# Kernel tuning notes

Measured on AMD Instinct MI355X. Metric: run time of the kernel, lower is better.

Reference implementation:

```python
import jax, jax.numpy as jnp
import numpy as np

B, S, HID, NH = 2, 2048, 2048, 16
HD = HID // NH  # 128
BASE = 10000.0


def rope_tables(seq_len, head_dim):
    inv_freq = 1.0 / (BASE ** (jnp.arange(0, head_dim, 2, dtype=jnp.float32) / head_dim))
    t = jnp.arange(seq_len, dtype=jnp.float32)
    freqs = jnp.einsum('i,j->ij', t, inv_freq)        # [s, d/2]
    emb = jnp.concatenate([freqs, freqs], axis=-1)     # [s, d]
    return jnp.cos(emb), jnp.sin(emb)


def apply_rotary(x, cos, sin):
    # x: [b, s, h, d]; cos/sin: [s, d]
    x1, x2 = x[..., ::2], x[..., 1::2]
    c = cos[None, :, None, ::2]
    s = sin[None, :, None, ::2]
    x1r = x1 * c - x2 * s
    x2r = x1 * s + x2 * c
    return jnp.stack([x1r, x2r], axis=-1).reshape(x.shape)


def setup_inputs() -> dict:
    key = jax.random.key(0)
    ks = jax.random.split(key, 5)
    scale = 1.0 / np.sqrt(HID)
    hidden_states = jax.random.normal(ks[0], (B, S, HID), jnp.float32)
    Wq = jax.random.normal(ks[1], (HID, HID), jnp.float32) * scale
    Wk = jax.random.normal(ks[2], (HID, HID), jnp.float32) * scale
    Wv = jax.random.normal(ks[3], (HID, HID), jnp.float32) * scale
    Wo = jax.random.normal(ks[4], (HID, HID), jnp.float32) * scale
    causal = jnp.tril(jnp.ones((S, S), dtype=bool))
    attention_mask = jnp.where(causal, 0.0, -1e9).astype(jnp.float32)[None, :, :]  # [1, S, S]
    return {'hidden_states': hidden_states, 'Wq': Wq, 'Wk': Wk, 'Wv': Wv,
            'Wo': Wo, 'attention_mask': attention_mask}


def reference(hidden_states, Wq, Wk, Wv, Wo, attention_mask):
    b, s, hid = hidden_states.shape
    q = (hidden_states @ Wq.T).reshape(b, s, NH, HD)
    k = (hidden_states @ Wk.T).reshape(b, s, NH, HD)
    v = (hidden_states @ Wv.T).reshape(b, s, NH, HD)
    cos, sin = rope_tables(s, HD)
    q = apply_rotary(q, cos, sin)
    k = apply_rotary(k, cos, sin)
    # [b, h, s, d]
    q = q.transpose(0, 2, 1, 3)
    k = k.transpose(0, 2, 1, 3)
    v = v.transpose(0, 2, 1, 3)
    scores = jnp.einsum('bhqd,bhkd->bhqk', q, k) / np.sqrt(HD).astype(np.float32)
    scores = scores + attention_mask[:, None, :, :]  # broadcast mask over heads
    probs = jax.nn.softmax(scores.astype(jnp.float32), axis=-1).astype(q.dtype)
    attn = jnp.einsum('bhqk,bhkd->bhqd', probs, v)
    attn = attn.transpose(0, 2, 1, 3).reshape(b, s, hid)
    return attn @ Wo.T
```

## Files before the change

kernel.cpp:

```cpp
#include <hip/hip_runtime.h>
#include <math.h>

typedef __attribute__((ext_vector_type(8))) short short8;
typedef __attribute__((ext_vector_type(4))) float f32x4;
typedef __attribute__((ext_vector_type(16))) float f32x16;
typedef __attribute__((ext_vector_type(4))) float fvec4;
typedef __attribute__((ext_vector_type(4))) unsigned short us4;
typedef __attribute__((ext_vector_type(2))) unsigned int uint2v;

#define DI __device__ __forceinline__
#define BARX asm volatile("s_barrier" ::: "memory")
#define WAITV6 asm volatile("s_waitcnt vmcnt(6)" ::: "memory")
#define WAITV4 asm volatile("s_waitcnt vmcnt(4)" ::: "memory")
#define WAITV0 asm volatile("s_waitcnt vmcnt(0)" ::: "memory")
#define WAITL0 asm volatile("s_waitcnt lgkmcnt(0)" ::: "memory")
#define SCHED0 __builtin_amdgcn_sched_barrier(0)

constexpr int BB = 2, SS = 2048, HIDc = 2048, NHc = 16, HDc = 128;
constexpr int MT = BB * SS;
constexpr int KC = HIDc;

constexpr size_t OFF_HB  = 0;
constexpr size_t OFF_WB  = OFF_HB + (size_t)MT * KC * 2;
constexpr size_t OFF_Q   = OFF_WB + (size_t)4 * HIDc * KC * 2;
constexpr size_t OFF_K   = OFF_Q  + (size_t)BB * NHc * SS * HDc * 2;
constexpr size_t OFF_V   = OFF_K  + (size_t)BB * NHc * SS * HDc * 2;
constexpr size_t OFF_ATT = OFF_V  + (size_t)BB * NHc * SS * HDc * 2;
constexpr size_t OFF_COS = OFF_ATT + (size_t)MT * HIDc * 2;
constexpr size_t OFF_SIN = OFF_COS + (size_t)SS * 32 * 4;
constexpr size_t WS_NEED = OFF_SIN + (size_t)SS * 32 * 4;

DI float bf2f(unsigned short u) { union { unsigned u; float f; } v; v.u = (unsigned)u << 16; return v.f; }
DI unsigned short f2bf(float f) {
  union { float f; unsigned u; } v; v.f = f;
  unsigned r = v.u + 0x7fffu + ((v.u >> 16) & 1u);
  return (unsigned short)(r >> 16);
}

DI void gload_lds16(const void* g, void* l) {
  __builtin_amdgcn_global_load_lds((const __attribute__((address_space(1))) void*)g,
                                   (__attribute__((address_space(3))) void*)l, 16, 0, 0);
}

DI unsigned cvtpk_bf16(float lo, float hi_) {
  unsigned r;
  asm("v_cvt_pk_bf16_f32 %0, %1, %2" : "=v"(r) : "v"(lo), "v"(hi_));
  return r;
}

__global__ void __launch_bounds__(256) cvt_kernel(
    const float* __restrict__ H,  const float* __restrict__ W0,
    const float* __restrict__ W1, const float* __restrict__ W2,
    const float* __restrict__ W3, unsigned short* __restrict__ dst,
    float* __restrict__ cosT, float* __restrict__ sinT)
{
  constexpr size_t HN = (size_t)MT * KC;
  constexpr size_t WN = (size_t)HIDc * KC;
  if (blockIdx.x >= 12288) {
    int idx = (blockIdx.x - 12288) * 256 + threadIdx.x;
    int t = idx >> 5, fi = idx & 31;
    float inv = powf(10000.0f, -(float)fi * (1.0f / 32.0f));
    float ang = (float)t * inv;
    cosT[idx] = cosf(ang);
    sinT[idx] = sinf(ang);
    return;
  }
  size_t e0 = ((size_t)blockIdx.x * 256 + threadIdx.x) * 8;
  const float* src; size_t off;
  if (e0 < HN) { src = H; off = e0; }
  else {
    size_t t = e0 - HN; int a = (int)(t >> 22);
    src = (a == 0) ? W0 : (a == 1) ? W1 : (a == 2) ? W2 : W3;
    off = t & (WN - 1);
  }
  fvec4 v0 = *(const fvec4*)(src + off);
  fvec4 v1 = *(const fvec4*)(src + off + 4);
  short8 o;
  o[0] = (short)f2bf(v0[0]); o[1] = (short)f2bf(v0[1]);
  o[2] = (short)f2bf(v0[2]); o[3] = (short)f2bf(v0[3]);
  o[4] = (short)f2bf(v1[0]); o[5] = (short)f2bf(v1[1]);
  o[6] = (short)f2bf(v1[2]); o[7] = (short)f2bf(v1[3]);
  *(short8*)(dst + e0) = o;
}

template<int NBX>
__global__ void __launch_bounds__(512, 2) gemm8p(
    const unsigned short* __restrict__ A,
    const unsigned short* __restrict__ Bw,
    void* __restrict__ dq, void* __restrict__ dk, void* __restrict__ dv,
    const float* __restrict__ cosT, const float* __restrict__ sinT)
{
  __shared__ __align__(16) unsigned short SL[8][128 * 64];
  const int tid = threadIdx.x, lane = tid & 63, w = tid >> 6;
  const int wm = w >> 2, wn = w & 3;
  const int ln15 = lane & 15, lq = lane >> 4;

  const int xcd = blockIdx.x & 7, idx = blockIdx.x >> 3;
  const int by = xcd * 2 + idx / NBX, bx = idx % NBX;
  const int m0 = by * 256, n0 = bx * 256;

  const int srow = tid >> 3;
  const int sc = (tid & 7) ^ (srow & 7);
  const unsigned short* Ab = A  + ((size_t)m0 + srow) * KC + sc * 8;
  const unsigned short* Bb = Bw + ((size_t)n0 + srow) * KC + sc * 8;

  constexpr int NT = KC / 64;
  auto stage = [&](int kt, bool isA, int half, int buf) {
    if (kt >= NT) return;
    const unsigned short* s = (isA ? Ab : Bb) + (size_t)(half * 128) * KC + kt * 64;
    int slot = (isA ? 0 : 4) + buf * 2 + half;
    unsigned short* d = &SL[slot][(size_t)(w * 64) * 8];
    gload_lds16(s, d);
    gload_lds16(s + (size_t)64 * KC, d + (size_t)512 * 8);
  };

  auto readA = [&](int buf, int q, int i, int ks) -> short8 {
    int rl = ((q & 1) << 6) + (i << 5) + (wm << 4) + ln15;
    return *(const short8*)&SL[buf * 2 + (q >> 1)]
        [rl * 64 + ((((ks << 2) + lq) ^ (rl & 7)) << 3)];
  };
  auto readB = [&](int buf, int j, int ks) -> short8 {
    int rl = ((wn & 1) << 6) + (j << 4) + ln15;
    return *(const short8*)&SL[4 + buf * 2 + (wn >> 1)]
        [rl * 64 + ((((ks << 2) + lq) ^ (rl & 7)) << 3)];
  };

  stage(0, true, 0, 0); stage(0, true, 1, 0);
  stage(0, false, 0, 0); stage(0, false, 1, 0);
  stage(1, false, 0, 1); stage(1, false, 1, 1); stage(1, true, 0, 1);
  WAITV6; BARX;

  f32x4 acc[8][4] = {};
  short8 bfr[4][2];
  constexpr int NIT = NT / 2;
  for (int t = 0; t < NIT; ++t) {
    const int k2 = 2 * t + 2, k3 = 2 * t + 3;
#pragma unroll
    for (int b = 0; b < 2; ++b) {
#pragma unroll
      for (int q = 0; q < 4; ++q) {
        short8 af[2][2];
#pragma unroll
        for (int i = 0; i < 2; ++i)
#pragma unroll
          for (int ks = 0; ks < 2; ++ks) af[i][ks] = readA(b, q, i, ks);
        if (q == 0) {
#pragma unroll
          for (int j = 0; j < 4; ++j)
#pragma unroll
            for (int ks = 0; ks < 2; ++ks) bfr[j][ks] = readB(b, j, ks);
        }
        if (b == 0) {
          if (q == 0) stage(2 * t + 1, true, 1, 1);
          else if (q == 1) stage(k2, false, 0, 0);
          else if (q == 2) stage(k2, false, 1, 0);
          else stage(k2, true, 0, 0);
        } else {
          if (q == 0) stage(k2, true, 1, 0);
          else if (q == 1) stage(k3, false, 0, 1);
          else if (q == 2) stage(k3, false, 1, 1);
          else stage(k3, true, 0, 1);
        }
        BARX;
        WAITL0; SCHED0;
        __builtin_amdgcn_s_setprio(1);
#pragma unroll
        for (int i = 0; i < 2; ++i)
#pragma unroll
          for (int j = 0; j < 4; ++j)
#pragma unroll
            for (int ks = 0; ks < 2; ++ks)
              acc[2 * q + i][j] = __builtin_amdgcn_mfma_f32_16x16x32_bf16(
                  af[i][ks], bfr[j][ks], acc[2 * q + i][j], 0, 0, 0);
        __builtin_amdgcn_s_setprio(0);
        if (q == 3) { if (t == NIT - 1) { WAITV0; } else { WAITV6; } }
        BARX;
      }
    }
  }

#pragma unroll
  for (int f = 0; f < 8; ++f)
#pragma unroll
    for (int j = 0; j < 4; ++j) {
      int col = n0 + wn * 64 + j * 16 + ln15;
      int z = col >> 11;
      int c2 = col & 2047;
      int h = c2 >> 7, d = c2 & 127;
      int m = m0 + 32 * f + 16 * wm + lq * 4;
      int b = m >> 11, s = m & 2047;
      if (z == 2) {
        us4 pk;
#pragma unroll
        for (int r = 0; r < 4; ++r) pk[r] = f2bf(acc[f][j][r]);
        *(us4*)((unsigned short*)dv + (((size_t)b * NHc + h) * HDc + d) * SS + s) = pk;
      } else {
        unsigned short* D = (unsigned short*)(z ? dk : dq);
        const int fi = (d >> 1) & 31;
        const bool odd = (d & 1) != 0;
#pragma unroll
        for (int r = 0; r < 4; ++r) {
          float v = acc[f][j][r];
          float p = __shfl_xor(v, 1);
          float cs = cosT[(size_t)(s + r) * 32 + fi];
          float sn = sinT[(size_t)(s + r) * 32 + fi];
          float y = odd ? (p * sn + v * cs) : (v * cs - p * sn);
          D[(((size_t)b * NHc + h) * SS + s + r) * HDc + d] = f2bf(y);
        }
      }
    }
}

template<int EPI, int NBX>
__global__ void __launch_bounds__(512, 2) gemm8(
    const unsigned short* __restrict__ A,
    const unsigned short* __restrict__ Bw,
    void* __restrict__ dq, void* __restrict__ dk, void* __restrict__ dv,
    const float* __restrict__ cosT, const float* __restrict__ sinT)
{
  __shared__ __align__(16) unsigned short Al[3][256 * 64];
  __shared__ __align__(16) unsigned short Bl[3][128 * 64];
  const int tid = threadIdx.x, lane = tid & 63, w = tid >> 6;
  const int wm = w >> 1, wn = w & 1;
  const int ln15 = lane & 15, lq = lane >> 4;

  const int xcd = blockIdx.x & 7, idx = blockIdx.x >> 3;
  const int by = xcd * 2 + idx / NBX, bx = idx % NBX;
  const int m0 = by * 256, n0 = bx * 128;

  const int srow = tid >> 3;
  const int sc = (tid & 7) ^ (srow & 7);
  const unsigned short* asrc[4];
  const unsigned short* bsrc[2];
#pragma unroll
  for (int l = 0; l < 4; ++l) asrc[l] = A  + (size_t)(m0 + l * 64 + srow) * KC + sc * 8;
#pragma unroll
  for (int l = 0; l < 2; ++l) bsrc[l] = Bw + (size_t)(n0 + l * 64 + srow) * KC + sc * 8;

  const int x7 = ln15 & 7;
  const int slA0 = (lq ^ x7) * 8;
  const int slA1 = ((4 + lq) ^ x7) * 8;
  int rA[4], rB[4];
#pragma unroll
  for (int i = 0; i < 4; ++i) rA[i] = (wm * 64 + i * 16 + ln15) * 64;
#pragma unroll
  for (int j = 0; j < 4; ++j) rB[j] = (wn * 64 + j * 16 + ln15) * 64;

  constexpr int NT = KC / 64;
  auto stA = [&](int kt, int buf, int l) {
    gload_lds16(asrc[l] + (size_t)kt * 64, &Al[buf][(size_t)(l * 512 + w * 64) * 8]);
  };
  auto stB = [&](int kt, int buf, int l) {
    gload_lds16(bsrc[l] + (size_t)kt * 64, &Bl[buf][(size_t)(l * 512 + w * 64) * 8]);
  };

  stA(0, 0, 0); stA(0, 0, 1); stA(0, 0, 2); stA(0, 0, 3); stB(0, 0, 0); stB(0, 0, 1);
  stA(1, 1, 0); stA(1, 1, 1); stA(1, 1, 2); stA(1, 1, 3); stB(1, 1, 0); stB(1, 1, 1);
  WAITV6; BARX;

  f32x4 acc[4][4] = {};
  int cb = 0, nb = 2;
  for (int kt = 0; kt < NT; ++kt) {
    const unsigned short* Ac = &Al[cb][0];
    const unsigned short* Bc = &Bl[cb][0];
    const bool pf = (kt + 2 < NT);
    short8 a01[2][2], a23[2][2], bf[4][2];

#pragma unroll
    for (int i = 0; i < 2; ++i) {
      a01[i][0] = *(const short8*)&Ac[rA[i] + slA0];
      a01[i][1] = *(const short8*)&Ac[rA[i] + slA1];
    }
#pragma unroll
    for (int j = 0; j < 4; ++j) {
      bf[j][0] = *(const short8*)&Bc[rB[j] + slA0];
      bf[j][1] = *(const short8*)&Bc[rB[j] + slA1];
    }
    if (pf) { stA(kt + 2, nb, 0); stA(kt + 2, nb, 1); stA(kt + 2, nb, 2); }
    BARX;
    WAITL0; SCHED0;
    __builtin_amdgcn_s_setprio(1);
#pragma unroll
    for (int i = 0; i < 2; ++i)
#pragma unroll
      for (int j = 0; j < 4; ++j)
#pragma unroll
        for (int k = 0; k < 2; ++k)
          acc[i][j] = __builtin_amdgcn_mfma_f32_16x16x32_bf16(a01[i][k], bf[j][k], acc[i][j], 0, 0, 0);
    __builtin_amdgcn_s_setprio(0);
    BARX;

#pragma unroll
    for (int i = 0; i < 2; ++i) {
      a23[i][0] = *(const short8*)&Ac[rA[2 + i] + slA0];
      a23[i][1] = *(const short8*)&Ac[rA[2 + i] + slA1];
    }
    if (pf) { stA(kt + 2, nb, 3); stB(kt + 2, nb, 0); stB(kt + 2, nb, 1); }
    BARX;
    WAITL0; SCHED0;
    __builtin_amdgcn_s_setprio(1);
#pragma unroll
    for (int i = 0; i < 2; ++i)
#pragma unroll
      for (int j = 0; j < 4; ++j)
#pragma unroll
        for (int k = 0; k < 2; ++k)
          acc[2 + i][j] = __builtin_amdgcn_mfma_f32_16x16x32_bf16(a23[i][k], bf[j][k], acc[2 + i][j], 0, 0, 0);
    __builtin_amdgcn_s_setprio(0);
    if (kt < NT - 2) { WAITV6; }
    else if (kt == NT - 2) { WAITV0; }
    BARX;

    cb = (cb == 2) ? 0 : cb + 1;
    nb = (nb == 2) ? 0 : nb + 1;
  }

  if (EPI == 1) {
    float* O = (float*)dq;
#pragma unroll
    for (int i = 0; i < 4; ++i)
#pragma unroll
      for (int j = 0; j < 4; ++j) {
        int col = n0 + wn * 64 + j * 16 + ln15;
        int m = m0 + wm * 64 + i * 16 + lq * 4;
#pragma unroll
        for (int r = 0; r < 4; ++r)
          O[(size_t)(m + r) * HIDc + col] = acc[i][j][r];
      }
  } else {
    unsigned short* V = (unsigned short*)dq;
#pragma unroll
    for (int i = 0; i < 4; ++i)
#pragma unroll
      for (int j = 0; j < 4; ++j) {
        int col = n0 + wn * 64 + j * 16 + ln15;
        int h = col >> 7, d = col & 127;
        int m = m0 + wm * 64 + i * 16 + lq * 4;
        int b = m >> 11, s = m & 2047;
        us4 pk;
#pragma unroll
        for (int r = 0; r < 4; ++r) pk[r] = f2bf(acc[i][j][r]);
        *(us4*)(V + (((size_t)b * NHc + h) * HDc + d) * SS + s) = pk;
      }
  }
}

__global__ void __launch_bounds__(512, 2) attn_kernel(
    const unsigned short* __restrict__ Qg,
    const unsigned short* __restrict__ Kg,
    const unsigned short* __restrict__ Vg,
    unsigned short* __restrict__ Og)
{
  __shared__ __align__(16) unsigned short Klds[3][64 * 128];
  __shared__ __align__(16) unsigned short Vlds[3][128 * 64];
  __shared__ __align__(16) unsigned short Plds[8][32 * 64];
  const int tid = threadIdx.x, lane = tid & 63, w = tid >> 6;
  const int l31 = lane & 31, hi = lane >> 5;

  const int wg = blockIdx.x;
  const int xcd = wg & 7, idx = wg >> 3;
  const int bh = xcd + 8 * (idx & 3);
  const int tt = idx >> 2;

  const int qtile = (w < 2) ? tt : (w < 4) ? (tt + 8) : (w < 6) ? (31 - tt) : (23 - tt);
  const int sub1 = w & 1;
  const int q0w = qtile * 64 + sub1 * 32;
  const int ntiles = 32 - tt;

  const size_t hbase = (size_t)bh * SS * HDc;
  const float CE = 1.44269504089f * 0.08838834764831845f;
  const int b = bh >> 4, h = bh & 15;

  short8 qf[8];
#pragma unroll
  for (int ks = 0; ks < 8; ++ks)
    qf[ks] = *(const short8*)(Qg + hbase + (size_t)(q0w + l31) * HDc + ks * 16 + hi * 8);

  f32x16 accO[4];
#pragma unroll
  for (int db = 0; db < 4; ++db)
#pragma unroll
    for (int r = 0; r < 16; ++r) accO[db][r] = 0.f;
  float mr = -1e30f, lr = 0.f;

  auto stage = [&](int kvt, int buf) {
    const int kv0 = kvt * 64;
#pragma unroll
    for (int p = 0; p < 2; ++p) {
      int c = p * 512 + tid;
      int krow = c >> 4, ksl = c & 15;
      gload_lds16(Kg + hbase + (size_t)(kv0 + krow) * HDc + ((ksl ^ (krow & 7)) << 3),
                  (unsigned short*)&Klds[buf][0] + (size_t)c * 8);
      int vd = c >> 3, vsl = c & 7;
      gload_lds16(Vg + hbase + (size_t)vd * SS + kv0 + ((vsl ^ (vd & 7)) << 3),
                  (unsigned short*)&Vlds[buf][0] + (size_t)c * 8);
    }
  };

  stage(0, 0); stage(1, 1);
  WAITV4; BARX;

  for (int kvt = 0; kvt < ntiles; ++kvt) {
    if (kvt + 2 < ntiles) stage(kvt + 2, (kvt + 2) % 3);
    const int cur = kvt % 3;

    if (kvt <= qtile) {
      const bool diag = (kvt == qtile);
      const bool haveT1 = (!diag) || sub1;

      f32x16 s0, s1;
#pragma unroll
      for (int r = 0; r < 16; ++r) s0[r] = 0.f;
      __builtin_amdgcn_s_setprio(1);
#pragma unroll
      for (int ks = 0; ks < 8; ++ks) {
        int row = l31;
        short8 kf = *(const short8*)&Klds[cur][row * 128 + (((2 * ks + hi) ^ (row & 7)) << 3)];
        s0 = __builtin_amdgcn_mfma_f32_32x32x16_bf16(kf, qf[ks], s0, 0, 0, 0);
      }
      if (haveT1) {
#pragma unroll
        for (int r = 0; r < 16; ++r) s1[r] = 0.f;
#pragma unroll
        for (int ks = 0; ks < 8; ++ks) {
          int row = 32 + l31;
          short8 kf = *(const short8*)&Klds[cur][row * 128 + (((2 * ks + hi) ^ (row & 7)) << 3)];
          s1 = __builtin_amdgcn_mfma_f32_32x32x16_bf16(kf, qf[ks], s1, 0, 0, 0);
        }
      }
      __builtin_amdgcn_s_setprio(0);

      if (diag) {
        if (sub1) {
#pragma unroll
          for (int r = 0; r < 16; ++r)
            if (((r & 3) + 8 * (r >> 2) + 4 * hi) > l31) s1[r] = -1e30f;
        } else {
#pragma unroll
          for (int r = 0; r < 16; ++r)
            if (((r & 3) + 8 * (r >> 2) + 4 * hi) > l31) s0[r] = -1e30f;
        }
      }

      float pmax = s0[0];
#pragma unroll
      for (int r = 1; r < 16; ++r) pmax = fmaxf(pmax, s0[r]);
      if (haveT1) {
#pragma unroll
        for (int r = 0; r < 16; ++r) pmax = fmaxf(pmax, s1[r]);
      }
      pmax = fmaxf(pmax, __shfl_xor(pmax, 32));

      int grow = (CE * (pmax - mr) > 8.0f) ? 1 : 0;
      if (__any(grow)) {
        float mn = fmaxf(mr, pmax);
        float al = exp2f(CE * (mr - mn));
        mr = mn; lr *= al;
        float alr[16];
#pragma unroll
        for (int r = 0; r < 16; ++r)
          alr[r] = __shfl(al, (r & 3) + 8 * (r >> 2) + 4 * hi);
#pragma unroll
        for (int db = 0; db < 4; ++db)
#pragma unroll
          for (int r = 0; r < 16; ++r) accO[db][r] *= alr[r];
      }

      float psum = 0.f;
#pragma unroll
      for (int r = 0; r < 16; ++r) {
        float p = exp2f(CE * (s0[r] - mr));
        s0[r] = p; psum += p;
      }
      if (haveT1) {
#pragma unroll
        for (int r = 0; r < 16; ++r) {
          float p = exp2f(CE * (s1[r] - mr));
          s1[r] = p; psum += p;
        }
      }
      psum += __shfl_xor(psum, 32);
      lr += psum;

#pragma unroll
      for (int i = 0; i < 4; ++i) {
        uint2v pk;
        pk[0] = cvtpk_bf16(s0[4 * i], s0[4 * i + 1]);
        pk[1] = cvtpk_bf16(s0[4 * i + 2], s0[4 * i + 3]);
        int chunk = i ^ (l31 & 7);
        *(uint2v*)&Plds[w][l31 * 64 + chunk * 8 + hi * 4] = pk;
      }
      if (haveT1) {
#pragma unroll
        for (int i = 0; i < 4; ++i) {
          uint2v pk;
          pk[0] = cvtpk_bf16(s1[4 * i], s1[4 * i + 1]);
          pk[1] = cvtpk_bf16(s1[4 * i + 2], s1[4 * i + 3]);
          int chunk = (4 + i) ^ (l31 & 7);
          *(uint2v*)&Plds[w][l31 * 64 + chunk * 8 + hi * 4] = pk;
        }
      }

      short8 ap[4];
#pragma unroll
      for (int ks = 0; ks < 2; ++ks)
        ap[ks] = *(const short8*)&Plds[w][l31 * 64 + (((2 * ks + hi) ^ (l31 & 7)) << 3)];
      if (haveT1) {
#pragma unroll
        for (int ks = 2; ks < 4; ++ks)
          ap[ks] = *(const short8*)&Plds[w][l31 * 64 + (((2 * ks + hi) ^ (l31 & 7)) << 3)];
      }

      __builtin_amdgcn_s_setprio(1);
#pragma unroll
      for (int db = 0; db < 4; ++db) {
        int row = db * 32 + l31;
#pragma unroll
        for (int ks = 0; ks < 2; ++ks) {
          short8 vf = *(const short8*)&Vlds[cur][row * 64 + (((2 * ks + hi) ^ (row & 7)) << 3)];
          accO[db] = __builtin_amdgcn_mfma_f32_32x32x16_bf16(ap[ks], vf, accO[db], 0, 0, 0);
        }
      }
      if (haveT1) {
#pragma unroll
        for (int db = 0; db < 4; ++db) {
          int row = db * 32 + l31;
#pragma unroll
          for (int ks = 2; ks < 4; ++ks) {
            short8 vf = *(const short8*)&Vlds[cur][row * 64 + (((2 * ks + hi) ^ (row & 7)) << 3)];
            accO[db] = __builtin_amdgcn_mfma_f32_32x32x16_bf16(ap[ks], vf, accO[db], 0, 0, 0);
          }
        }
      }
      __builtin_amdgcn_s_setprio(0);
    }

    if (kvt < ntiles - 2) { WAITV4; } else { WAITV0; }
    BARX;
  }

  float il = 1.0f / lr;
  float ilr[16];
#pragma unroll
  for (int r = 0; r < 16; ++r)
    ilr[r] = __shfl(il, (r & 3) + 8 * (r >> 2) + 4 * hi);
#pragma unroll
  for (int db = 0; db < 4; ++db)
#pragma unroll
    for (int r = 0; r < 16; ++r) {
      int q = q0w + (r & 3) + 8 * (r >> 2) + 4 * hi;
      int d = db * 32 + l31;
      Og[((size_t)b * SS + q) * HIDc + h * HDc + d] = f2bf(accO[db][r] * ilr[r]);
    }
}

extern "C" void kernel_launch(void* const* d_in, const int* in_sizes, int n_in,
                              void* d_out, int out_size, void* d_ws, size_t ws_size,
                              hipStream_t stream)
{
  if (ws_size < WS_NEED) return;

  const float* H  = (const float*)d_in[0];
  const float* Wq = (const float*)d_in[1];
  const float* Wk = (const float*)d_in[2];
  const float* Wv = (const float*)d_in[3];
  const float* Wo = (const float*)d_in[4];
  char* ws = (char*)d_ws;
  unsigned short* HB = (unsigned short*)(ws + OFF_HB);
  unsigned short* WB = (unsigned short*)(ws + OFF_WB);
  unsigned short* Qb = (unsigned short*)(ws + OFF_Q);
  unsigned short* Kb = (unsigned short*)(ws + OFF_K);
  unsigned short* Vb = (unsigned short*)(ws + OFF_V);
  unsigned short* AT = (unsigned short*)(ws + OFF_ATT);
  float* cosT = (float*)(ws + OFF_COS);
  float* sinT = (float*)(ws + OFF_SIN);

  cvt_kernel<<<12544, 256, 0, stream>>>(H, Wq, Wk, Wv, Wo, HB, cosT, sinT);
  gemm8p<16><<<256, 512, 0, stream>>>(HB, WB, Qb, Kb, Vb, cosT, sinT);
  gemm8<2, 16><<<256, 512, 0, stream>>>(HB, WB + (size_t)2 * HIDc * KC,
                                        Vb, nullptr, nullptr, nullptr, nullptr);
  attn_kernel<<<256, 512, 0, stream>>>(Qb, Kb, Vb, AT);
  gemm8<1, 16><<<256, 512, 0, stream>>>(AT, WB + (size_t)3 * HIDc * KC,
                                        d_out, nullptr, nullptr, nullptr, nullptr);
}
```

Before: 243.6 us.

## Stage 128-row KV tiles double-buffered and split P@V into 32-column halves

```diff
diff --git a/kernel.cpp b/kernel.cpp
--- a/kernel.cpp
+++ b/kernel.cpp
@@ -11,7 +11,6 @@
 #define DI __device__ __forceinline__
 #define BARX asm volatile("s_barrier" ::: "memory")
 #define WAITV6 asm volatile("s_waitcnt vmcnt(6)" ::: "memory")
-#define WAITV4 asm volatile("s_waitcnt vmcnt(4)" ::: "memory")
 #define WAITV0 asm volatile("s_waitcnt vmcnt(0)" ::: "memory")
 #define WAITL0 asm volatile("s_waitcnt lgkmcnt(0)" ::: "memory")
 #define SCHED0 __builtin_amdgcn_sched_barrier(0)
@@ -351,9 +350,9 @@
     const unsigned short* __restrict__ Vg,
     unsigned short* __restrict__ Og)
 {
-  __shared__ __align__(16) unsigned short Klds[3][64 * 128];
-  __shared__ __align__(16) unsigned short Vlds[3][128 * 64];
-  __shared__ __align__(16) unsigned short Plds[8][32 * 64];
+  __shared__ __align__(16) unsigned short Klds[2][128 * 128];
+  __shared__ __align__(16) unsigned short Vlds[2][128 * 128];
+  __shared__ __align__(16) unsigned short Plds[8][32 * 32];
   const int tid = threadIdx.x, lane = tid & 63, w = tid >> 6;
   const int l31 = lane & 31, hi = lane >> 5;
 
@@ -365,7 +364,7 @@
   const int qtile = (w < 2) ? tt : (w < 4) ? (tt + 8) : (w < 6) ? (31 - tt) : (23 - tt);
   const int sub1 = w & 1;
   const int q0w = qtile * 64 + sub1 * 32;
-  const int ntiles = 32 - tt;
+  const int NT128 = (33 - tt) >> 1;
 
   const size_t hbase = (size_t)bh * SS * HDc;
   const float CE = 1.44269504089f * 0.08838834764831845f;
@@ -383,160 +382,157 @@
     for (int r = 0; r < 16; ++r) accO[db][r] = 0.f;
   float mr = -1e30f, lr = 0.f;
 
-  auto stage = [&](int kvt, int buf) {
-    const int kv0 = kvt * 64;
-#pragma unroll
-    for (int p = 0; p < 2; ++p) {
+  auto stage = [&](int T, int buf) {
+    const int kv0 = T * 128;
+#pragma unroll
+    for (int p = 0; p < 4; ++p) {
       int c = p * 512 + tid;
       int krow = c >> 4, ksl = c & 15;
       gload_lds16(Kg + hbase + (size_t)(kv0 + krow) * HDc + ((ksl ^ (krow & 7)) << 3),
                   (unsigned short*)&Klds[buf][0] + (size_t)c * 8);
-      int vd = c >> 3, vsl = c & 7;
+      int vd = c >> 4, vsl = c & 15;
       gload_lds16(Vg + hbase + (size_t)vd * SS + kv0 + ((vsl ^ (vd & 7)) << 3),
                   (unsigned short*)&Vlds[buf][0] + (size_t)c * 8);
     }
   };
 
-  stage(0, 0); stage(1, 1);
-  WAITV4; BARX;
-
-  for (int kvt = 0; kvt < ntiles; ++kvt) {
-    if (kvt + 2 < ntiles) stage(kvt + 2, (kvt + 2) % 3);
-    const int cur = kvt % 3;
-
-    if (kvt <= qtile) {
-      const bool diag = (kvt == qtile);
-      const bool haveT1 = (!diag) || sub1;
-
-      f32x16 s0, s1;
-#pragma unroll
-      for (int r = 0; r < 16; ++r) s0[r] = 0.f;
-      __builtin_amdgcn_s_setprio(1);
-#pragma unroll
-      for (int ks = 0; ks < 8; ++ks) {
-        int row = l31;
-        short8 kf = *(const short8*)&Klds[cur][row * 128 + (((2 * ks + hi) ^ (row & 7)) << 3)];
-        s0 = __builtin_amdgcn_mfma_f32_32x32x16_bf16(kf, qf[ks], s0, 0, 0, 0);
-      }
-      if (haveT1) {
-#pragma unroll
-        for (int r = 0; r < 16; ++r) s1[r] = 0.f;
+  stage(0, 0);
+  WAITV0; BARX;
+
+  for (int T = 0; T < NT128; ++T) {
+    const int cur = T & 1;
+    if (T + 1 < NT128) stage(T + 1, cur ^ 1);
+
+#pragma unroll
+    for (int sub = 0; sub < 2; ++sub) {
+      const int kvt = 2 * T + sub;
+      if (kvt <= qtile) {
+        const bool diag = (kvt == qtile);
+        const bool haveT1 = (!diag) || sub1;
+
+        f32x16 s0, s1;
+#pragma unroll
+        for (int r = 0; r < 16; ++r) s0[r] = 0.f;
+        __builtin_amdgcn_s_setprio(1);
 #pragma unroll
         for (int ks = 0; ks < 8; ++ks) {
-          int row = 32 + l31;
+          int row = sub * 64 + l31;
           short8 kf = *(const short8*)&Klds[cur][row * 128 + (((2 * ks + hi) ^ (row & 7)) << 3)];
-          s1 = __builtin_amdgcn_mfma_f32_32x32x16_bf16(kf, qf[ks], s1, 0, 0, 0);
-        }
-      }
-      __builtin_amdgcn_s_setprio(0);
-
-      if (diag) {
-        if (sub1) {
+          s0 = __builtin_amdgcn_mfma_f32_32x32x16_bf16(kf, qf[ks], s0, 0, 0, 0);
+        }
+        if (haveT1) {
+#pragma unroll
+          for (int r = 0; r < 16; ++r) s1[r] = 0.f;
+#pragma unroll
+          for (int ks = 0; ks < 8; ++ks) {
+            int row = sub * 64 + 32 + l31;
+            short8 kf = *(const short8*)&Klds[cur][row * 128 + (((2 * ks + hi) ^ (row & 7)) << 3)];
+            s1 = __builtin_amdgcn_mfma_f32_32x32x16_bf16(kf, qf[ks], s1, 0, 0, 0);
+          }
+        }
+        __builtin_amdgcn_s_setprio(0);
+
+        if (diag) {
+          if (sub1) {
+#pragma unroll
+            for (int r = 0; r < 16; ++r)
+              if (((r & 3) + 8 * (r >> 2) + 4 * hi) > l31) s1[r] = -1e30f;
+          } else {
+#pragma unroll
+            for (int r = 0; r < 16; ++r)
+              if (((r & 3) + 8 * (r >> 2) + 4 * hi) > l31) s0[r] = -1e30f;
+          }
+        }
+
+        float pmax = s0[0];
+#pragma unroll
+        for (int r = 1; r < 16; ++r) pmax = fmaxf(pmax, s0[r]);
+        if (haveT1) {
+#pragma unroll
+          for (int r = 0; r < 16; ++r) pmax = fmaxf(pmax, s1[r]);
+        }
+        pmax = fmaxf(pmax, __shfl_xor(pmax, 32));
+
+        int grow = (CE * (pmax - mr) > 8.0f) ? 1 : 0;
+        if (__any(grow)) {
+          float mn = fmaxf(mr, pmax);
+          float al = exp2f(CE * (mr - mn));
+          mr = mn; lr *= al;
+          float alr[16];
 #pragma unroll
           for (int r = 0; r < 16; ++r)
-            if (((r & 3) + 8 * (r >> 2) + 4 * hi) > l31) s1[r] = -1e30f;
-        } else {
-#pragma unroll
-          for (int r = 0; r < 16; ++r)
-            if (((r & 3) + 8 * (r >> 2) + 4 * hi) > l31) s0[r] = -1e30f;
-        }
-      }
-
-      float pmax = s0[0];
-#pragma unroll
-      for (int r = 1; r < 16; ++r) pmax = fmaxf(pmax, s0[r]);
-      if (haveT1) {
-#pragma unroll
-        for (int r = 0; r < 16; ++r) pmax = fmaxf(pmax, s1[r]);
-      }
-      pmax = fmaxf(pmax, __shfl_xor(pmax, 32));
-
-      int grow = (CE * (pmax - mr) > 8.0f) ? 1 : 0;
-      if (__any(grow)) {
-        float mn = fmaxf(mr, pmax);
-        float al = exp2f(CE * (mr - mn));
-        mr = mn; lr *= al;
-        float alr[16];
-#pragma unroll
-        for (int r = 0; r < 16; ++r)
-          alr[r] = __shfl(al, (r & 3) + 8 * (r >> 2) + 4 * hi);
-#pragma unroll
-        for (int db = 0; db < 4; ++db)
-#pragma unroll
-          for (int r = 0; r < 16; ++r) accO[db][r] *= alr[r];
-      }
-
-      float psum = 0.f;
-#pragma unroll
-      for (int r = 0; r < 16; ++r) {
-        float p = exp2f(CE * (s0[r] - mr));
-        s0[r] = p; psum += p;
-      }
-      if (haveT1) {
+            alr[r] = __shfl(al, (r & 3) + 8 * (r >> 2) + 4 * hi);
+#pragma unroll
+          for (int db = 0; db < 4; ++db)
+#pragma unroll
+            for (int r = 0; r < 16; ++r) accO[db][r] *= alr[r];
+        }
+
+        float psum = 0.f;
 #pragma unroll
         for (int r = 0; r < 16; ++r) {
-          float p = exp2f(CE * (s1[r] - mr));
-          s1[r] = p; psum += p;
-        }
-      }
-      psum += __shfl_xor(psum, 32);
-      lr += psum;
-
-#pragma unroll
-      for (int i = 0; i < 4; ++i) {
-        uint2v pk;
-        pk[0] = cvtpk_bf16(s0[4 * i], s0[4 * i + 1]);
-        pk[1] = cvtpk_bf16(s0[4 * i + 2], s0[4 * i + 3]);
-        int chunk = i ^ (l31 & 7);
-        *(uint2v*)&Plds[w][l31 * 64 + chunk * 8 + hi * 4] = pk;
-      }
-      if (haveT1) {
+          float p = exp2f(CE * (s0[r] - mr));
+          s0[r] = p; psum += p;
+        }
+        if (haveT1) {
+#pragma unroll
+          for (int r = 0; r < 16; ++r) {
+            float p = exp2f(CE * (s1[r] - mr));
+            s1[r] = p; psum += p;
+          }
+        }
+        psum += __shfl_xor(psum, 32);
+        lr += psum;
+
 #pragma unroll
         for (int i = 0; i < 4; ++i) {
           uint2v pk;
-          pk[0] = cvtpk_bf16(s1[4 * i], s1[4 * i + 1]);
-          pk[1] = cvtpk_bf16(s1[4 * i + 2], s1[4 * i + 3]);
-          int chunk = (4 + i) ^ (l31 & 7);
-          *(uint2v*)&Plds[w][l31 * 64 + chunk * 8 + hi * 4] = pk;
+          pk[0] = cvtpk_bf16(s0[4 * i], s0[4 * i + 1]);
+          pk[1] = cvtpk_bf16(s0[4 * i + 2], s0[4 * i + 3]);
+          int c = i ^ (l31 & 3);
+          *(uint2v*)&Plds[w][l31 * 32 + c * 8 + hi * 4] = pk;
+        }
+        {
+          short8 ap0 = *(const short8*)&Plds[w][l31 * 32 + ((hi ^ (l31 & 3)) << 3)];
+          short8 ap1 = *(const short8*)&Plds[w][l31 * 32 + (((2 + hi) ^ (l31 & 3)) << 3)];
+          __builtin_amdgcn_s_setprio(1);
+#pragma unroll
+          for (int db = 0; db < 4; ++db) {
+            int row = db * 32 + l31;
+            short8 vf0 = *(const short8*)&Vlds[cur][row * 128 + ((sub * 8 + ((0 + hi) ^ (row & 7))) << 3)];
+            short8 vf1 = *(const short8*)&Vlds[cur][row * 128 + ((sub * 8 + ((2 + hi) ^ (row & 7))) << 3)];
+            accO[db] = __builtin_amdgcn_mfma_f32_32x32x16_bf16(ap0, vf0, accO[db], 0, 0, 0);
+            accO[db] = __builtin_amdgcn_mfma_f32_32x32x16_bf16(ap1, vf1, accO[db], 0, 0, 0);
+          }
+          __builtin_amdgcn_s_setprio(0);
+        }
+
+        if (haveT1) {
+#pragma unroll
+          for (int i = 0; i < 4; ++i) {
+            uint2v pk;
+            pk[0] = cvtpk_bf16(s1[4 * i], s1[4 * i + 1]);
+            pk[1] = cvtpk_bf16(s1[4 * i + 2], s1[4 * i + 3]);
+            int c = i ^ (l31 & 3);
+            *(uint2v*)&Plds[w][l31 * 32 + c * 8 + hi * 4] = pk;
+          }
+          short8 ap0 = *(const short8*)&Plds[w][l31 * 32 + ((hi ^ (l31 & 3)) << 3)];
+          short8 ap1 = *(const short8*)&Plds[w][l31 * 32 + (((2 + hi) ^ (l31 & 3)) << 3)];
+          __builtin_amdgcn_s_setprio(1);
+#pragma unroll
+          for (int db = 0; db < 4; ++db) {
+            int row = db * 32 + l31;
+            short8 vf0 = *(const short8*)&Vlds[cur][row * 128 + ((sub * 8 + ((4 + hi) ^ (row & 7))) << 3)];
+            short8 vf1 = *(const short8*)&Vlds[cur][row * 128 + ((sub * 8 + ((6 + hi) ^ (row & 7))) << 3)];
+            accO[db] = __builtin_amdgcn_mfma_f32_32x32x16_bf16(ap0, vf0, accO[db], 0, 0, 0);
+            accO[db] = __builtin_amdgcn_mfma_f32_32x32x16_bf16(ap1, vf1, accO[db], 0, 0, 0);
+          }
+          __builtin_amdgcn_s_setprio(0);
         }
       }
-
-      short8 ap[4];
-#pragma unroll
-      for (int ks = 0; ks < 2; ++ks)
-        ap[ks] = *(const short8*)&Plds[w][l31 * 64 + (((2 * ks + hi) ^ (l31 & 7)) << 3)];
-      if (haveT1) {
-#pragma unroll
-        for (int ks = 2; ks < 4; ++ks)
-          ap[ks] = *(const short8*)&Plds[w][l31 * 64 + (((2 * ks + hi) ^ (l31 & 7)) << 3)];
-      }
-
-      __builtin_amdgcn_s_setprio(1);
-#pragma unroll
-      for (int db = 0; db < 4; ++db) {
-        int row = db * 32 + l31;
-#pragma unroll
-        for (int ks = 0; ks < 2; ++ks) {
-          short8 vf = *(const short8*)&Vlds[cur][row * 64 + (((2 * ks + hi) ^ (row & 7)) << 3)];
-          accO[db] = __builtin_amdgcn_mfma_f32_32x32x16_bf16(ap[ks], vf, accO[db], 0, 0, 0);
-        }
-      }
-      if (haveT1) {
-#pragma unroll
-        for (int db = 0; db < 4; ++db) {
-          int row = db * 32 + l31;
-#pragma unroll
-          for (int ks = 2; ks < 4; ++ks) {
-            short8 vf = *(const short8*)&Vlds[cur][row * 64 + (((2 * ks + hi) ^ (row & 7)) << 3)];
-            accO[db] = __builtin_amdgcn_mfma_f32_32x32x16_bf16(ap[ks], vf, accO[db], 0, 0, 0);
-          }
-        }
-      }
-      __builtin_amdgcn_s_setprio(0);
-    }
-
-    if (kvt < ntiles - 2) { WAITV4; } else { WAITV0; }
-    BARX;
+    }
+
+    WAITV0; BARX;
   }
 
   float il = 1.0f / lr;
```

After: 238.5 us. -2.1%, faster.
